# Kernel optimization log

Hardware: AMD Instinct MI355X
Metric: run time of the kernel (lower is better)

The kernel has to match this reference:

```python
import jax, jax.numpy as jnp
import numpy as np

B, L, V, D_MODEL = 1, 2048, 32000, 768
N_LAYER, D_STATE, EXPAND, D_CONV = 2, 16, 2, 4
D_INNER = EXPAND * D_MODEL            # 1536
DT_RANK = -(-D_MODEL // D_STATE)      # ceil(768/16) = 48
EPS = 1e-5


def setup_inputs() -> dict:
    key = jax.random.key(0)
    ks = jax.random.split(key, 12)
    s = 0.02
    inp = {
        "input_ids": jax.random.randint(ks[0], (B, L), 0, V),
        "emb": jax.random.normal(ks[1], (V, D_MODEL), jnp.float32) * s,
        "norm_w": jnp.ones((N_LAYER, D_MODEL), jnp.float32),
        "in_proj_w": jax.random.normal(ks[2], (N_LAYER, D_MODEL, 2 * D_INNER), jnp.float32) * s,
        "conv_w": jax.random.normal(ks[3], (N_LAYER, D_INNER, 1, D_CONV), jnp.float32) * s,
        "conv_b": jnp.zeros((N_LAYER, D_INNER), jnp.float32),
        "x_proj_w": jax.random.normal(ks[4], (N_LAYER, D_INNER, DT_RANK + 2 * D_STATE), jnp.float32) * s,
        "dt_proj_w": jax.random.normal(ks[5], (N_LAYER, DT_RANK, D_INNER), jnp.float32) * s,
        "dt_proj_b": jax.random.normal(ks[6], (N_LAYER, D_INNER), jnp.float32) * s,
        "A_log": jnp.tile(jnp.log(jnp.arange(1, D_STATE + 1, dtype=jnp.float32)), (N_LAYER, D_INNER, 1)),
        "D": jnp.ones((N_LAYER, D_INNER), jnp.float32),
        "out_proj_w": jax.random.normal(ks[7], (N_LAYER, D_INNER, D_MODEL), jnp.float32) * s,
    }
    return inp


def _rmsnorm(x, w):
    return x * jax.lax.rsqrt(jnp.mean(x * x, axis=-1, keepdims=True) + EPS) * w


def _selective_scan(u, delta, A, Bm, Cm, D):
    # u, delta: (b,l,d); A: (d,n); Bm, Cm: (b,l,n); D: (d,)
    deltaA = jnp.exp(delta[..., None] * A)                     # (b,l,d,n)
    dBu = delta[..., None] * Bm[:, :, None, :] * u[..., None]  # (b,l,d,n)

    def comb(c1, c2):
        a1, b1 = c1
        a2, b2 = c2
        return a2 * a1, a2 * b1 + b2

    _, h = jax.lax.associative_scan(comb, (deltaA, dBu), axis=1)
    y = jnp.einsum('bldn,bln->bld', h, Cm)
    return y + u * D


def _mamba_block(x, in_proj_w, conv_w, conv_b, x_proj_w, dt_proj_w, dt_proj_b, A_log, D, out_proj_w):
    # x: (b,l,d_model)
    xz = x @ in_proj_w                                  # (b,l,2*d_inner)
    xr, res = jnp.split(xz, 2, axis=-1)
    # causal depthwise conv1d (left pad d_conv-1)
    xc = jax.lax.conv_general_dilated(
        jnp.swapaxes(xr, 1, 2), conv_w, (1,), [(D_CONV - 1, 0)],
        feature_group_count=D_INNER,
        dimension_numbers=('NCH', 'OIH', 'NCH'))
    xr = jax.nn.silu(jnp.swapaxes(xc + conv_b[:, None], 1, 2))  # (b,l,d_inner)

    A = -jnp.exp(A_log)                                 # (d_inner, n)
    x_dbl = xr @ x_proj_w                               # (b,l,dt_rank+2n)
    dt, Bm, Cm = jnp.split(x_dbl, [DT_RANK, DT_RANK + D_STATE], axis=-1)
    delta = jax.nn.softplus(dt @ dt_proj_w + dt_proj_b) # (b,l,d_inner)
    y = _selective_scan(xr, delta, A, Bm, Cm, D)
    return (y * jax.nn.silu(res)) @ out_proj_w


def reference(input_ids, emb, norm_w, in_proj_w, conv_w, conv_b, x_proj_w,
              dt_proj_w, dt_proj_b, A_log, D, out_proj_w):
    x = emb[input_ids]                                  # (b,l,d_model)
    for i in range(N_LAYER):
        x = x + _mamba_block(_rmsnorm(x, norm_w[i]), in_proj_w[i], conv_w[i],
                             conv_b[i], x_proj_w[i], dt_proj_w[i], dt_proj_b[i],
                             A_log[i], D[i], out_proj_w[i])
    return x
```

## Files before the change

### kernel.cpp

```cpp
#include <hip/hip_runtime.h>
#include <math.h>

#define L_SEQ 2048
#define DM    768
#define DI    1536
#define DTR   48
#define DST   16
#define XDW   80
#define NCH   64
#define LC    32
#define XPS   8
#define XPK   (DI / XPS)
#define XPAD  200

typedef short bf16x8 __attribute__((ext_vector_type(8)));
typedef float f32x4  __attribute__((ext_vector_type(4)));

__device__ __forceinline__ float silu_f(float x) {
    return x / (1.0f + __expf(-x));
}

__device__ __forceinline__ short f2bf(float x) {
    union { float f; unsigned u; } v; v.f = x;
    unsigned r = v.u + 0x7fff + ((v.u >> 16) & 1);
    return (short)(r >> 16);
}

__device__ __forceinline__ float bf2f(short s) {
    union { float f; unsigned u; } v;
    v.u = ((unsigned)(unsigned short)s) << 16;
    return v.f;
}

__global__ __launch_bounds__(256) void prep_kernel(
    const int*   __restrict__ ids,
    const float* __restrict__ emb,
    const float* __restrict__ norm_w,
    const float* __restrict__ in_proj_w,
    const float* __restrict__ out_proj_w,
    const float* __restrict__ x_proj_w,
    float* __restrict__ x,
    short* __restrict__ xn_bf,
    short* __restrict__ ipw_t, short* __restrict__ opw_t, short* __restrict__ xpw_t)
{
    __shared__ float tile[32 * 33];
    __shared__ float wred[4];
    const int tid = threadIdx.x;

    {
        int row = blockIdx.x;
        int tok = ids[row];
        float4 v4 = make_float4(0.f, 0.f, 0.f, 0.f);
        if (tid < DM / 4) {
            v4 = ((const float4*)emb)[(size_t)tok * (DM / 4) + tid];
            ((float4*)x)[(size_t)row * (DM / 4) + tid] = v4;
        }
        float s = v4.x * v4.x + v4.y * v4.y + v4.z * v4.z + v4.w * v4.w;
        #pragma unroll
        for (int off = 32; off > 0; off >>= 1) s += __shfl_down(s, off, 64);
        int wave = tid >> 6, lane = tid & 63;
        if (lane == 0) wred[wave] = s;
        __syncthreads();
        float tot = wred[0] + wred[1] + wred[2] + wred[3];
        float rs = rsqrtf(tot / (float)DM + 1e-5f);
        if (tid < DM / 4) {
            int i = tid * 4;
            short4 o;
            o.x = f2bf(v4.x * rs * norm_w[i + 0]);
            o.y = f2bf(v4.y * rs * norm_w[i + 1]);
            o.z = f2bf(v4.z * rs * norm_w[i + 2]);
            o.w = f2bf(v4.w * rs * norm_w[i + 3]);
            ((short4*)xn_bf)[(size_t)row * (DM / 4) + tid] = o;
        }
        __syncthreads();
    }

    int lx = tid & 31, ly = tid >> 5;
    for (int t = blockIdx.x; t < 7200; t += gridDim.x) {
        int layer = t >= 3600;
        int tt = t - layer * 3600;
        const float* src; short* dst; int K, N, txc;
        if (tt < 2304) {
            src = in_proj_w + (size_t)layer * DM * 2 * DI;
            dst = ipw_t + (size_t)layer * 2 * DI * DM;
            K = DM; N = 2 * DI; txc = 96;
        } else if (tt < 3456) {
            tt -= 2304;
            src = out_proj_w + (size_t)layer * DI * DM;
            dst = opw_t + (size_t)layer * DM * DI;
            K = DI; N = DM; txc = 24;
        } else {
            tt -= 3456;
            src = x_proj_w + (size_t)layer * DI * XDW;
            dst = xpw_t + (size_t)layer * XDW * DI;
            K = DI; N = XDW; txc = 3;
        }
        int n0 = (tt % txc) * 32, k0 = (tt / txc) * 32;
        __syncthreads();
        #pragma unroll
        for (int i = 0; i < 4; i++) {
            int nn = n0 + lx;
            tile[(ly + i * 8) * 33 + lx] =
                (nn < N) ? src[(size_t)(k0 + ly + i * 8) * N + nn] : 0.f;
        }
        __syncthreads();
        #pragma unroll
        for (int i = 0; i < 4; i++) {
            int nn = n0 + ly + i * 8;
            if (nn < N)
                dst[(size_t)nn * K + k0 + lx] = f2bf(tile[lx * 33 + ly + i * 8]);
        }
    }
}

__global__ __launch_bounds__(256) void rmsnorm_kernel(
    const float* __restrict__ x, const float* __restrict__ w,
    short* __restrict__ out)
{
    int row = blockIdx.x;
    const float* xr = x + (size_t)row * DM;
    float s = 0.f;
    for (int i = threadIdx.x; i < DM; i += 256) { float v = xr[i]; s += v * v; }
    #pragma unroll
    for (int off = 32; off > 0; off >>= 1) s += __shfl_down(s, off, 64);
    __shared__ float ws[4];
    int wave = threadIdx.x >> 6, lane = threadIdx.x & 63;
    if (lane == 0) ws[wave] = s;
    __syncthreads();
    float tot = ws[0] + ws[1] + ws[2] + ws[3];
    float rs = rsqrtf(tot / (float)DM + 1e-5f);
    for (int i = threadIdx.x; i < DM; i += 256)
        out[(size_t)row * DM + i] = f2bf(xr[i] * rs * w[i]);
}

__global__ __launch_bounds__(256) void gemm_bf16_bt(
    const short* __restrict__ A, const short* __restrict__ Bt,
    float* __restrict__ C, int M, int N, int K)
{
    __shared__ short As[128 * 32];
    __shared__ short Bs[128 * 32];
    int tid = threadIdx.x, lane = tid & 63, w = tid >> 6;
    int wr = w >> 1, wc = w & 1;
    int brow = blockIdx.y * 128, bcol = blockIdx.x * 128;

    f32x4 acc[4][4] = {};

    for (int k0 = 0; k0 < K; k0 += 32) {
        #pragma unroll
        for (int i = 0; i < 2; i++) {
            int c = tid + i * 256;
            int r = c >> 2, q = c & 3;
            const short* ga = A  + (size_t)(brow + r) * K + k0 + q * 8;
            const short* gb = Bt + (size_t)(bcol + r) * K + k0 + q * 8;
            __builtin_amdgcn_global_load_lds(
                (const __attribute__((address_space(1))) void*)ga,
                (__attribute__((address_space(3))) void*)&As[r * 32 + q * 8],
                16, 0, 0);
            __builtin_amdgcn_global_load_lds(
                (const __attribute__((address_space(1))) void*)gb,
                (__attribute__((address_space(3))) void*)&Bs[r * 32 + q * 8],
                16, 0, 0);
        }
        __syncthreads();

        bf16x8 af[4], bfv[4];
        int kh = (lane >> 4) * 8;
        int ml = lane & 15;
        #pragma unroll
        for (int t = 0; t < 4; t++) {
            af[t]  = *(const bf16x8*)&As[(wr * 64 + t * 16 + ml) * 32 + kh];
            bfv[t] = *(const bf16x8*)&Bs[(wc * 64 + t * 16 + ml) * 32 + kh];
        }
        #pragma unroll
        for (int mt = 0; mt < 4; mt++)
            #pragma unroll
            for (int nt = 0; nt < 4; nt++)
                acc[mt][nt] = __builtin_amdgcn_mfma_f32_16x16x32_bf16(
                    af[mt], bfv[nt], acc[mt][nt], 0, 0, 0);
        __syncthreads();
    }

    int r0 = (lane >> 4) * 4, c0 = lane & 15;
    #pragma unroll
    for (int mt = 0; mt < 4; mt++)
        #pragma unroll
        for (int nt = 0; nt < 4; nt++)
            #pragma unroll
            for (int reg = 0; reg < 4; reg++) {
                int row = brow + wr * 64 + mt * 16 + r0 + reg;
                int col = bcol + wc * 64 + nt * 16 + c0;
                C[(size_t)row * N + col] = acc[mt][nt][reg];
            }
}

__global__ __launch_bounds__(256) void gemm_bf16_bt_n64(
    const short* __restrict__ A, const short* __restrict__ Bt,
    float* __restrict__ C, int M, int N, int K)
{
    __shared__ short As[128 * 32];
    __shared__ short Bs[64 * 32];
    int tid = threadIdx.x, lane = tid & 63, w = tid >> 6;
    int brow = blockIdx.y * 128, bcol = blockIdx.x * 64;

    f32x4 acc[2][4] = {};

    for (int k0 = 0; k0 < K; k0 += 32) {
        #pragma unroll
        for (int i = 0; i < 2; i++) {
            int c = tid + i * 256;
            int r = c >> 2, q = c & 3;
            const short* ga = A + (size_t)(brow + r) * K + k0 + q * 8;
            __builtin_amdgcn_global_load_lds(
                (const __attribute__((address_space(1))) void*)ga,
                (__attribute__((address_space(3))) void*)&As[r * 32 + q * 8],
                16, 0, 0);
        }
        {
            int r = tid >> 2, q = tid & 3;
            const short* gb = Bt + (size_t)(bcol + r) * K + k0 + q * 8;
            __builtin_amdgcn_global_load_lds(
                (const __attribute__((address_space(1))) void*)gb,
                (__attribute__((address_space(3))) void*)&Bs[r * 32 + q * 8],
                16, 0, 0);
        }
        __syncthreads();

        bf16x8 af[2], bfv[4];
        int kh = (lane >> 4) * 8;
        int ml = lane & 15;
        #pragma unroll
        for (int mt = 0; mt < 2; mt++)
            af[mt] = *(const bf16x8*)&As[(w * 32 + mt * 16 + ml) * 32 + kh];
        #pragma unroll
        for (int nt = 0; nt < 4; nt++)
            bfv[nt] = *(const bf16x8*)&Bs[(nt * 16 + ml) * 32 + kh];
        #pragma unroll
        for (int mt = 0; mt < 2; mt++)
            #pragma unroll
            for (int nt = 0; nt < 4; nt++)
                acc[mt][nt] = __builtin_amdgcn_mfma_f32_16x16x32_bf16(
                    af[mt], bfv[nt], acc[mt][nt], 0, 0, 0);
        __syncthreads();
    }

    int r0 = (lane >> 4) * 4, c0 = lane & 15;
    #pragma unroll
    for (int mt = 0; mt < 2; mt++)
        #pragma unroll
        for (int nt = 0; nt < 4; nt++)
            #pragma unroll
            for (int reg = 0; reg < 4; reg++) {
                int row = brow + w * 32 + mt * 16 + r0 + reg;
                int col = bcol + nt * 16 + c0;
                C[(size_t)row * N + col] += acc[mt][nt][reg];
            }
}

__global__ __launch_bounds__(256) void convxproj_kernel(
    const float* __restrict__ xz, const float* __restrict__ cw,
    const float* __restrict__ cb, const short* __restrict__ xpw_t,
    short* __restrict__ xr_bf, float* __restrict__ part)
{
    __shared__ __align__(16) short lds[64 * XPAD];
    const int tid = threadIdx.x;
    int rg = blockIdx.x;
    int sp = blockIdx.y;
    int l0 = rg * 64;
    int k0 = sp * XPK;

    for (int e = tid; e < 64 * XPK; e += 256) {
        int ll = e / XPK, cc = e % XPK;
        int l = l0 + ll, c = k0 + cc;
        float4 wc4 = ((const float4*)cw)[c];
        const float* col = xz + c;
        float acc = cb[c];
        if (l >= 3) {
            acc += wc4.x * col[(size_t)(l - 3) * (2 * DI)]
                 + wc4.y * col[(size_t)(l - 2) * (2 * DI)]
                 + wc4.z * col[(size_t)(l - 1) * (2 * DI)]
                 + wc4.w * col[(size_t)l * (2 * DI)];
        } else {
            const float wv[4] = {wc4.x, wc4.y, wc4.z, wc4.w};
            for (int k = 0; k < 4; k++) {
                int ls = l - 3 + k;
                if (ls >= 0) acc += wv[k] * col[(size_t)ls * (2 * DI)];
            }
        }
        short b = f2bf(silu_f(acc));
        lds[ll * XPAD + cc] = b;
        xr_bf[(size_t)l * DI + c] = b;
    }
    __syncthreads();

    int w = tid >> 6, lane = tid & 63;
    int ml = lane & 15, kh = (lane >> 4) * 8;
    int rl = w * 16 + ml;
    f32x4 acc5[5] = {};
    for (int ks = 0; ks < XPK; ks += 32) {
        bf16x8 a = *(const bf16x8*)&lds[rl * XPAD + ks + kh];
        #pragma unroll
        for (int t5 = 0; t5 < 5; t5++) {
            bf16x8 b = *(const bf16x8*)&xpw_t[(size_t)(t5 * 16 + ml) * DI + k0 + ks + kh];
            acc5[t5] = __builtin_amdgcn_mfma_f32_16x16x32_bf16(a, b, acc5[t5], 0, 0, 0);
        }
    }
    float* po = part + (size_t)sp * L_SEQ * XDW;
    int rb = l0 + w * 16 + (lane >> 4) * 4;
    #pragma unroll
    for (int t5 = 0; t5 < 5; t5++)
        #pragma unroll
        for (int reg = 0; reg < 4; reg++)
            po[(size_t)(rb + reg) * XDW + t5 * 16 + ml] = acc5[t5][reg];
}

__global__ __launch_bounds__(256) void dtproj_fused(
    const float* __restrict__ xpart, const float* __restrict__ dpw,
    const float* __restrict__ dpb, float* __restrict__ delta,
    float* __restrict__ xdbl_bc)
{
    __shared__ __align__(16) float As_f[16 * 68];
    __shared__ __align__(16) float Bs_f[16 * 68];
    int tid = threadIdx.x;
    int ty = tid >> 4, tx = tid & 15;
    int t = blockIdx.x;
    int bcol = (t % 24) * 64;
    int brow = (t / 24) * 64;

    float acc[4][4] = {};
    for (int k0 = 0; k0 < 48; k0 += 16) {
        __syncthreads();
        #pragma unroll
        for (int i = 0; i < 4; i++) {
            int idx = tid + i * 256;
            int m = idx >> 4, k = idx & 15;
            float s = 0.f;
            #pragma unroll
            for (int p = 0; p < XPS; p++)
                s += xpart[((size_t)p * L_SEQ + brow + m) * XDW + k0 + k];
            As_f[k * 68 + m] = s;
        }
        #pragma unroll
        for (int i = 0; i < 4; i++) {
            int idx = tid + i * 256;
            int k = idx >> 6, n = idx & 63;
            Bs_f[k * 68 + n] = dpw[(size_t)(k0 + k) * DI + bcol + n];
        }
        __syncthreads();
        #pragma unroll
        for (int k = 0; k < 16; k++) {
            float4 av = *(const float4*)&As_f[k * 68 + ty * 4];
            float4 bv = *(const float4*)&Bs_f[k * 68 + tx * 4];
            float a4[4] = {av.x, av.y, av.z, av.w};
            float b4[4] = {bv.x, bv.y, bv.z, bv.w};
            #pragma unroll
            for (int i = 0; i < 4; i++)
                #pragma unroll
                for (int jj = 0; jj < 4; jj++)
                    acc[i][jj] += a4[i] * b4[jj];
        }
    }
    #pragma unroll
    for (int i = 0; i < 4; i++) {
        int row = brow + ty * 4 + i;
        #pragma unroll
        for (int jj = 0; jj < 4; jj++) {
            int col = bcol + tx * 4 + jj;
            float v = acc[i][jj] + dpb[col];
            delta[(size_t)row * DI + col] = (v > 20.f) ? v : log1pf(__expf(v));
        }
    }
    if (t % 24 == 0) {
        for (int e = tid; e < 64 * 32; e += 256) {
            int r = e >> 5, cc = e & 31;
            float s = 0.f;
            #pragma unroll
            for (int p = 0; p < XPS; p++)
                s += xpart[((size_t)p * L_SEQ + brow + r) * XDW + DTR + cc];
            xdbl_bc[(size_t)(brow + r) * 32 + cc] = s;
        }
    }
}

__global__ __launch_bounds__(256) void scan_passA(
    const float* __restrict__ delta, const short* __restrict__ xr_bf,
    const float* __restrict__ xdbl_bc, const float* __restrict__ al,
    float* __restrict__ aprod, float* __restrict__ hfin)
{
    int d = blockIdx.x * 256 + threadIdx.x;
    int c = blockIdx.y;

    float Aloc[DST], h[DST], P[DST];
    #pragma unroll
    for (int n4 = 0; n4 < DST; n4 += 4) {
        float4 alv = *(const float4*)&al[(size_t)d * DST + n4];
        Aloc[n4 + 0] = -__expf(alv.x); Aloc[n4 + 1] = -__expf(alv.y);
        Aloc[n4 + 2] = -__expf(alv.z); Aloc[n4 + 3] = -__expf(alv.w);
    }
    #pragma unroll
    for (int n = 0; n < DST; n++) { h[n] = 0.f; P[n] = 1.f; }

    int l0 = c * LC;
    for (int l = l0; l < l0 + LC; l++) {
        float dl = delta[(size_t)l * DI + d];
        float ul = bf2f(xr_bf[(size_t)l * DI + d]);
        float du = dl * ul;
        float Bv[DST];
        const float4* B4 = (const float4*)(xdbl_bc + (size_t)l * 32);
        *(float4*)&Bv[0] = B4[0]; *(float4*)&Bv[4]  = B4[1];
        *(float4*)&Bv[8] = B4[2]; *(float4*)&Bv[12] = B4[3];
        #pragma unroll
        for (int n = 0; n < DST; n++) {
            float da = __expf(dl * Aloc[n]);
            h[n] = h[n] * da + du * Bv[n];
            P[n] *= da;
        }
    }
    size_t base = ((size_t)c * DI + d) * DST;
    #pragma unroll
    for (int n = 0; n < DST; n += 4) {
        *(float4*)&aprod[base + n] = *(float4*)&P[n];
        *(float4*)&hfin[base + n]  = *(float4*)&h[n];
    }
}

__global__ __launch_bounds__(256) void scan_passB(
    const float* __restrict__ aprod, const float* __restrict__ hfin,
    float* __restrict__ hin)
{
    int idx = blockIdx.x * 256 + threadIdx.x;
    if (idx >= DI * DST) return;
    float cur = 0.f;
    for (int c = 0; c < NCH; c++) {
        size_t o = (size_t)c * DI * DST + idx;
        hin[o] = cur;
        cur = hfin[o] + aprod[o] * cur;
    }
}

__global__ __launch_bounds__(256) void scan_passC(
    const float* __restrict__ delta, const short* __restrict__ xr_bf,
    const float* __restrict__ xdbl_bc, const float* __restrict__ al,
    const float* __restrict__ dpp, const float* __restrict__ hin,
    const float* __restrict__ xz, short* __restrict__ y2)
{
    int d = blockIdx.x * 256 + threadIdx.x;
    int c = blockIdx.y;

    float Aloc[DST], h[DST];
    #pragma unroll
    for (int n4 = 0; n4 < DST; n4 += 4) {
        float4 alv = *(const float4*)&al[(size_t)d * DST + n4];
        Aloc[n4 + 0] = -__expf(alv.x); Aloc[n4 + 1] = -__expf(alv.y);
        Aloc[n4 + 2] = -__expf(alv.z); Aloc[n4 + 3] = -__expf(alv.w);
    }
    size_t base = ((size_t)c * DI + d) * DST;
    #pragma unroll
    for (int n = 0; n < DST; n += 4)
        *(float4*)&h[n] = *(const float4*)&hin[base + n];
    float Dd = dpp[d];

    int l0 = c * LC;
    for (int l = l0; l < l0 + LC; l++) {
        float dl = delta[(size_t)l * DI + d];
        float ul = bf2f(xr_bf[(size_t)l * DI + d]);
        float du = dl * ul;
        float Bv[DST], Cv[DST];
        const float4* B4 = (const float4*)(xdbl_bc + (size_t)l * 32);
        const float4* C4 = (const float4*)(xdbl_bc + (size_t)l * 32 + 16);
        *(float4*)&Bv[0] = B4[0]; *(float4*)&Bv[4]  = B4[1];
        *(float4*)&Bv[8] = B4[2]; *(float4*)&Bv[12] = B4[3];
        *(float4*)&Cv[0] = C4[0]; *(float4*)&Cv[4]  = C4[1];
        *(float4*)&Cv[8] = C4[2]; *(float4*)&Cv[12] = C4[3];
        float y = 0.f;
        #pragma unroll
        for (int n = 0; n < DST; n++) {
            float da = __expf(dl * Aloc[n]);
            h[n] = h[n] * da + du * Bv[n];
            y += h[n] * Cv[n];
        }
        y += ul * Dd;
        float r = xz[(size_t)l * (2 * DI) + DI + d];
        y2[(size_t)l * DI + d] = f2bf(y * silu_f(r));
    }
}

extern "C" void kernel_launch(void* const* d_in, const int* in_sizes, int n_in,
                              void* d_out, int out_size, void* d_ws, size_t ws_size,
                              hipStream_t stream)
{
    const int*   ids       = (const int*)d_in[0];
    const float* emb       = (const float*)d_in[1];
    const float* norm_w    = (const float*)d_in[2];
    const float* in_proj_w = (const float*)d_in[3];
    const float* conv_w    = (const float*)d_in[4];
    const float* conv_b    = (const float*)d_in[5];
    const float* x_proj_w  = (const float*)d_in[6];
    const float* dt_proj_w = (const float*)d_in[7];
    const float* dt_proj_b = (const float*)d_in[8];
    const float* A_log     = (const float*)d_in[9];
    const float* Dp        = (const float*)d_in[10];
    const float* out_proj_w= (const float*)d_in[11];

    float* x = (float*)d_out;

    char* wsb = (char*)d_ws;
    auto alloc_f = [&](size_t n) { float* p = (float*)wsb; wsb += n * 4; return p; };
    auto alloc_s = [&](size_t n) { short* p = (short*)wsb; wsb += ((n * 2 + 15) & ~15ull); return p; };

    float* xz      = alloc_f((size_t)L_SEQ * 2 * DI);
    float* delta   = alloc_f((size_t)L_SEQ * DI);
    float* xpart   = alloc_f((size_t)XPS * L_SEQ * XDW);
    float* xdbl_bc = alloc_f((size_t)L_SEQ * 32);
    float* aprod   = alloc_f((size_t)NCH * DI * DST);
    float* hfin    = alloc_f((size_t)NCH * DI * DST);
    float* hin     = alloc_f((size_t)NCH * DI * DST);
    short* xn_bf   = alloc_s((size_t)L_SEQ * DM);
    short* y2_bf   = alloc_s((size_t)L_SEQ * DI);
    short* xr_bf   = alloc_s((size_t)L_SEQ * DI);
    short* ipw_t   = alloc_s((size_t)2 * 2 * DI * DM);
    short* opw_t   = alloc_s((size_t)2 * DM * DI);
    short* xpw_t   = alloc_s((size_t)2 * XDW * DI);

    prep_kernel<<<L_SEQ, 256, 0, stream>>>(
        ids, emb, norm_w, in_proj_w, out_proj_w, x_proj_w,
        x, xn_bf, ipw_t, opw_t, xpw_t);

    for (int layer = 0; layer < 2; layer++) {
        const float* nw   = norm_w    + (size_t)layer * DM;
        const float* cw   = conv_w    + (size_t)layer * DI * 4;
        const float* cb   = conv_b    + (size_t)layer * DI;
        const float* dpw  = dt_proj_w + (size_t)layer * DTR * DI;
        const float* dpb  = dt_proj_b + (size_t)layer * DI;
        const float* al   = A_log     + (size_t)layer * DI * DST;
        const float* dpp  = Dp        + (size_t)layer * DI;
        const short* ipwt = ipw_t + (size_t)layer * 2 * DI * DM;
        const short* opwt = opw_t + (size_t)layer * DM * DI;
        const short* xpwt = xpw_t + (size_t)layer * XDW * DI;

        if (layer == 1)
            rmsnorm_kernel<<<L_SEQ, 256, 0, stream>>>(x, nw, xn_bf);

        gemm_bf16_bt<<<dim3(2 * DI / 128, L_SEQ / 128), 256, 0, stream>>>(
            xn_bf, ipwt, xz, L_SEQ, 2 * DI, DM);

        convxproj_kernel<<<dim3(32, XPS), 256, 0, stream>>>(
            xz, cw, cb, xpwt, xr_bf, xpart);

        dtproj_fused<<<768, 256, 0, stream>>>(xpart, dpw, dpb, delta, xdbl_bc);

        scan_passA<<<dim3(DI / 256, NCH), 256, 0, stream>>>(
            delta, xr_bf, xdbl_bc, al, aprod, hfin);
        scan_passB<<<(DI * DST) / 256, 256, 0, stream>>>(aprod, hfin, hin);
        scan_passC<<<dim3(DI / 256, NCH), 256, 0, stream>>>(
            delta, xr_bf, xdbl_bc, al, dpp, hin, xz, y2_bf);

        gemm_bf16_bt_n64<<<dim3(DM / 64, L_SEQ / 128), 256, 0, stream>>>(
            y2_bf, opwt, x, L_SEQ, DM, DI);
    }
}
```

Before: 513.6 us.

## Emit bf16 in_proj outputs split into conv and gate buffers; unfuse conv from x_proj

The in_proj GEMM now writes bf16 into two separate buffers, one for the conv input and one for the residual gate, replacing the single fp32 xz tensor. This halves the bytes written by the GEMM and later read by the conv and scan. The fused conv+x_proj kernel is split into an elementwise conv/SiLU kernel and a separate split-K x_proj MFMA kernel that reads xr_bf from global memory, which adds a launch and a round trip through global memory. Rounding the pre-conv activations and the gate to bf16 reduces precision.

```diff
diff --git a/kernel.cpp b/kernel.cpp
--- a/kernel.cpp
+++ b/kernel.cpp
@@ -11,7 +11,6 @@
 #define LC    32
 #define XPS   8
 #define XPK   (DI / XPS)
-#define XPAD  200
 
 typedef short bf16x8 __attribute__((ext_vector_type(8)));
 typedef float f32x4  __attribute__((ext_vector_type(4)));
@@ -133,9 +132,9 @@
         out[(size_t)row * DM + i] = f2bf(xr[i] * rs * w[i]);
 }
 
-__global__ __launch_bounds__(256) void gemm_bf16_bt(
+__global__ __launch_bounds__(256) void gemm_inproj(
     const short* __restrict__ A, const short* __restrict__ Bt,
-    float* __restrict__ C, int M, int N, int K)
+    short* __restrict__ xcz_bf, short* __restrict__ res_bf, int M, int N, int K)
 {
     __shared__ short As[128 * 32];
     __shared__ short Bs[128 * 32];
@@ -180,6 +179,8 @@
         __syncthreads();
     }
 
+    short* dst  = (bcol < DI) ? xcz_bf : res_bf;
+    int    cofs = (bcol < DI) ? bcol : (bcol - DI);
     int r0 = (lane >> 4) * 4, c0 = lane & 15;
     #pragma unroll
     for (int mt = 0; mt < 4; mt++)
@@ -188,8 +189,8 @@
             #pragma unroll
             for (int reg = 0; reg < 4; reg++) {
                 int row = brow + wr * 64 + mt * 16 + r0 + reg;
-                int col = bcol + wc * 64 + nt * 16 + c0;
-                C[(size_t)row * N + col] = acc[mt][nt][reg];
+                int col = cofs + wc * 64 + nt * 16 + c0;
+                dst[(size_t)row * DI + col] = f2bf(acc[mt][nt][reg]);
             }
 }
 
@@ -256,61 +257,57 @@
             }
 }
 
-__global__ __launch_bounds__(256) void convxproj_kernel(
-    const float* __restrict__ xz, const float* __restrict__ cw,
-    const float* __restrict__ cb, const short* __restrict__ xpw_t,
-    short* __restrict__ xr_bf, float* __restrict__ part)
-{
-    __shared__ __align__(16) short lds[64 * XPAD];
-    const int tid = threadIdx.x;
-    int rg = blockIdx.x;
-    int sp = blockIdx.y;
-    int l0 = rg * 64;
-    int k0 = sp * XPK;
-
-    for (int e = tid; e < 64 * XPK; e += 256) {
-        int ll = e / XPK, cc = e % XPK;
-        int l = l0 + ll, c = k0 + cc;
-        float4 wc4 = ((const float4*)cw)[c];
-        const float* col = xz + c;
-        float acc = cb[c];
-        if (l >= 3) {
-            acc += wc4.x * col[(size_t)(l - 3) * (2 * DI)]
-                 + wc4.y * col[(size_t)(l - 2) * (2 * DI)]
-                 + wc4.z * col[(size_t)(l - 1) * (2 * DI)]
-                 + wc4.w * col[(size_t)l * (2 * DI)];
-        } else {
-            const float wv[4] = {wc4.x, wc4.y, wc4.z, wc4.w};
-            for (int k = 0; k < 4; k++) {
-                int ls = l - 3 + k;
-                if (ls >= 0) acc += wv[k] * col[(size_t)ls * (2 * DI)];
-            }
-        }
-        short b = f2bf(silu_f(acc));
-        lds[ll * XPAD + cc] = b;
-        xr_bf[(size_t)l * DI + c] = b;
-    }
-    __syncthreads();
-
-    int w = tid >> 6, lane = tid & 63;
+__global__ __launch_bounds__(256) void conv_silu_kernel(
+    const short* __restrict__ xcz_bf, const float* __restrict__ w,
+    const float* __restrict__ b, short* __restrict__ xr_bf)
+{
+    int idx = blockIdx.x * 256 + threadIdx.x;
+    if (idx >= L_SEQ * DI) return;
+    int l = idx / DI, c = idx % DI;
+    float4 wc = ((const float4*)w)[c];
+    const short* col = xcz_bf + c;
+    float acc = b[c];
+    if (l >= 3) {
+        acc += wc.x * bf2f(col[(size_t)(l - 3) * DI])
+             + wc.y * bf2f(col[(size_t)(l - 2) * DI])
+             + wc.z * bf2f(col[(size_t)(l - 1) * DI])
+             + wc.w * bf2f(col[(size_t)l * DI]);
+    } else {
+        const float wv[4] = {wc.x, wc.y, wc.z, wc.w};
+        for (int k = 0; k < 4; k++) {
+            int ls = l - 3 + k;
+            if (ls >= 0) acc += wv[k] * bf2f(col[(size_t)ls * DI]);
+        }
+    }
+    xr_bf[idx] = f2bf(silu_f(acc));
+}
+
+__global__ __launch_bounds__(256) void xproj_splitk(
+    const short* __restrict__ xr_bf,
+    const short* __restrict__ xpw_t,
+    float* __restrict__ part)
+{
+    int w = threadIdx.x >> 6, lane = threadIdx.x & 63;
+    int r0 = blockIdx.x * 64 + w * 16;
+    int k0 = blockIdx.y * XPK;
     int ml = lane & 15, kh = (lane >> 4) * 8;
-    int rl = w * 16 + ml;
-    f32x4 acc5[5] = {};
+
+    f32x4 acc[5] = {};
     for (int ks = 0; ks < XPK; ks += 32) {
-        bf16x8 a = *(const bf16x8*)&lds[rl * XPAD + ks + kh];
-        #pragma unroll
-        for (int t5 = 0; t5 < 5; t5++) {
-            bf16x8 b = *(const bf16x8*)&xpw_t[(size_t)(t5 * 16 + ml) * DI + k0 + ks + kh];
-            acc5[t5] = __builtin_amdgcn_mfma_f32_16x16x32_bf16(a, b, acc5[t5], 0, 0, 0);
-        }
-    }
-    float* po = part + (size_t)sp * L_SEQ * XDW;
-    int rb = l0 + w * 16 + (lane >> 4) * 4;
-    #pragma unroll
-    for (int t5 = 0; t5 < 5; t5++)
+        bf16x8 a = *(const bf16x8*)&xr_bf[(size_t)(r0 + ml) * DI + k0 + ks + kh];
+        #pragma unroll
+        for (int t = 0; t < 5; t++) {
+            bf16x8 b = *(const bf16x8*)&xpw_t[(size_t)(t * 16 + ml) * DI + k0 + ks + kh];
+            acc[t] = __builtin_amdgcn_mfma_f32_16x16x32_bf16(a, b, acc[t], 0, 0, 0);
+        }
+    }
+    float* po = part + (size_t)blockIdx.y * L_SEQ * XDW;
+    int r_base = r0 + (lane >> 4) * 4;
+    #pragma unroll
+    for (int t = 0; t < 5; t++)
         #pragma unroll
         for (int reg = 0; reg < 4; reg++)
-            po[(size_t)(rb + reg) * XDW + t5 * 16 + ml] = acc5[t5][reg];
+            po[(size_t)(r_base + reg) * XDW + t * 16 + ml] = acc[t][reg];
 }
 
 __global__ __launch_bounds__(256) void dtproj_fused(
@@ -441,7 +438,7 @@
     const float* __restrict__ delta, const short* __restrict__ xr_bf,
     const float* __restrict__ xdbl_bc, const float* __restrict__ al,
     const float* __restrict__ dpp, const float* __restrict__ hin,
-    const float* __restrict__ xz, short* __restrict__ y2)
+    const short* __restrict__ res_bf, short* __restrict__ y2)
 {
     int d = blockIdx.x * 256 + threadIdx.x;
     int c = blockIdx.y;
@@ -479,7 +476,7 @@
             y += h[n] * Cv[n];
         }
         y += ul * Dd;
-        float r = xz[(size_t)l * (2 * DI) + DI + d];
+        float r = bf2f(res_bf[(size_t)l * DI + d]);
         y2[(size_t)l * DI + d] = f2bf(y * silu_f(r));
     }
 }
@@ -507,13 +504,14 @@
     auto alloc_f = [&](size_t n) { float* p = (float*)wsb; wsb += n * 4; return p; };
     auto alloc_s = [&](size_t n) { short* p = (short*)wsb; wsb += ((n * 2 + 15) & ~15ull); return p; };
 
-    float* xz      = alloc_f((size_t)L_SEQ * 2 * DI);
     float* delta   = alloc_f((size_t)L_SEQ * DI);
     float* xpart   = alloc_f((size_t)XPS * L_SEQ * XDW);
     float* xdbl_bc = alloc_f((size_t)L_SEQ * 32);
     float* aprod   = alloc_f((size_t)NCH * DI * DST);
     float* hfin    = alloc_f((size_t)NCH * DI * DST);
     float* hin     = alloc_f((size_t)NCH * DI * DST);
+    short* xcz_bf  = alloc_s((size_t)L_SEQ * DI);
+    short* res_bf  = alloc_s((size_t)L_SEQ * DI);
     short* xn_bf   = alloc_s((size_t)L_SEQ * DM);
     short* y2_bf   = alloc_s((size_t)L_SEQ * DI);
     short* xr_bf   = alloc_s((size_t)L_SEQ * DI);
@@ -540,11 +538,13 @@
         if (layer == 1)
             rmsnorm_kernel<<<L_SEQ, 256, 0, stream>>>(x, nw, xn_bf);
 
-        gemm_bf16_bt<<<dim3(2 * DI / 128, L_SEQ / 128), 256, 0, stream>>>(
-            xn_bf, ipwt, xz, L_SEQ, 2 * DI, DM);
-
-        convxproj_kernel<<<dim3(32, XPS), 256, 0, stream>>>(
-            xz, cw, cb, xpwt, xr_bf, xpart);
+        gemm_inproj<<<dim3(2 * DI / 128, L_SEQ / 128), 256, 0, stream>>>(
+            xn_bf, ipwt, xcz_bf, res_bf, L_SEQ, 2 * DI, DM);
+
+        conv_silu_kernel<<<(L_SEQ * DI) / 256, 256, 0, stream>>>(
+            xcz_bf, cw, cb, xr_bf);
+
+        xproj_splitk<<<dim3(L_SEQ / 64, XPS), 256, 0, stream>>>(xr_bf, xpwt, xpart);
 
         dtproj_fused<<<768, 256, 0, stream>>>(xpart, dpw, dpb, delta, xdbl_bc);
 
@@ -552,7 +552,7 @@
             delta, xr_bf, xdbl_bc, al, aprod, hfin);
         scan_passB<<<(DI * DST) / 256, 256, 0, stream>>>(aprod, hfin, hin);
         scan_passC<<<dim3(DI / 256, NCH), 256, 0, stream>>>(
-            delta, xr_bf, xdbl_bc, al, dpp, hin, xz, y2_bf);
+            delta, xr_bf, xdbl_bc, al, dpp, hin, res_bf, y2_bf);
 
         gemm_bf16_bt_n64<<<dim3(DM / 64, L_SEQ / 128), 256, 0, stream>>>(
             y2_bf, opwt, x, L_SEQ, DM, DI);
```

Result: faster. 468.4 us (-8.8%).
